# Kernel optimization log

Measured on AMD Instinct MI355X. Metric: run time of the kernel, lower is better.

The kernel has to match this reference:

```python
import jax, jax.numpy as jnp
import numpy as np

B, N, EG = 4, 16384, 131072
H, DK, DV, DM = 4, 32, 32, 128


def setup_inputs() -> dict:
    key = jax.random.key(0)
    ks = jax.random.split(key, 12)
    s = 0.05
    return {
        "edge_indices": jax.random.randint(ks[0], (B, 2, EG), 0, N, dtype=jnp.int32),
        "edge_features": jax.random.normal(ks[1], (B, EG, DM), jnp.float32),
        "input_Q": jax.random.normal(ks[2], (B, N, DM), jnp.float32),
        "input_K": jax.random.normal(ks[3], (B, N, DM), jnp.float32),
        "input_V": jax.random.normal(ks[4], (B, N, DM), jnp.float32),
        "W_Q": jax.random.normal(ks[5], (DM, H * DK), jnp.float32) * s,
        "W_K": jax.random.normal(ks[6], (DM, H * DK), jnp.float32) * s,
        "W_V": jax.random.normal(ks[7], (DM, H * DV), jnp.float32) * s,
        "W_E": jax.random.normal(ks[8], (DM, H * DV), jnp.float32) * s,
        "W_fc": jax.random.normal(ks[9], (H * DV, DM), jnp.float32) * s,
        "ln_gamma": jnp.ones((DM,), jnp.float32),
        "ln_beta": jnp.zeros((DM,), jnp.float32),
    }


def _layer_norm(x, g, b, eps=1e-5):
    mu = jnp.mean(x, axis=-1, keepdims=True)
    var = jnp.mean(jnp.square(x - mu), axis=-1, keepdims=True)
    return g * (x - mu) * jax.lax.rsqrt(var + eps) + b


def _proj(x, W, d):
    # [B, T, DM] @ [DM, H*d] -> [B, H, T, d]
    bsz, t, _ = x.shape
    return (x @ W).reshape(bsz, t, H, d).transpose(0, 2, 1, 3)


def reference(edge_indices, edge_features, input_Q, input_K, input_V,
              W_Q, W_K, W_V, W_E, W_fc, ln_gamma, ln_beta):
    residual = input_Q
    bsz, n_nodes, _ = input_Q.shape
    Q = _proj(input_Q, W_Q, DK)        # [B,H,N,dk]
    K = _proj(input_K, W_K, DK)
    V = _proj(input_V, W_V, DV)
    E = _proj(edge_features, W_E, DV)  # [B,H,Eg,dv]

    inv_sqrt_dk = 1.0 / np.sqrt(DK).astype(np.float32)

    def one_graph(Qb, Kb, Vb, Eb, idx):
        src, tgt = idx[0], idx[1]                       # [Eg]
        Qe = Qb[:, src]                                  # [H,Eg,dk]
        Ke = Kb[:, tgt]
        Ve = Vb[:, tgt]
        scores = (Qe * Ke) * inv_sqrt_dk * Eb            # [H,Eg,dv]
        attn = jnp.exp(jnp.clip(scores.sum(-1, keepdims=True), -5.0, 5.0))  # [H,Eg,1]
        msg = attn * Ve                                  # [H,Eg,dv]
        num = jnp.zeros((H, n_nodes, DV), Qb.dtype).at[:, src].add(msg)
        den = jnp.zeros((H, n_nodes, 1), Qb.dtype).at[:, src].add(attn)
        return num / (den + 1e-8), attn

    out, attn = jax.vmap(one_graph)(Q, K, V, E, edge_indices)  # [B,H,N,dv], [B,H,Eg,1]

    out = out.transpose(0, 2, 1, 3).reshape(bsz, n_nodes, H * DV)
    out = out @ W_fc
    out = _layer_norm(out + residual, ln_gamma, ln_beta)
    # torch code returns attn from the last batch iteration (leading dim 1)
    return out, attn[-1:]
```

## Files before the change

kernel.cpp:

```cpp
#include <hip/hip_runtime.h>

#define BB 4
#define NN 16384
#define EGc 131072
#define CAP 64
#define INVSQ 0.17677669529663687f

typedef unsigned int uint;
typedef unsigned short ushort;
typedef short short8 __attribute__((ext_vector_type(8)));
typedef float floatx4 __attribute__((ext_vector_type(4)));

__device__ __forceinline__ float bflo(uint u) { return __uint_as_float(u << 16); }
__device__ __forceinline__ float bfhi(uint u) { return __uint_as_float(u & 0xffff0000u); }
__device__ __forceinline__ ushort f2bf(float f) {
    uint u = __float_as_uint(f);
    u += 0x7fffu + ((u >> 16) & 1u);
    return (ushort)(u >> 16);
}

#define SA_STRIDE 136
#define SW_STRIDE 136
#define SY_STRIDE 132
struct __align__(16) SMem {
    union {
        struct {
            ushort sA[64 * SA_STRIDE];
            ushort sW[128 * SW_STRIDE];
        };
        float  sY[64 * SY_STRIDE];
        ushort sOut[64 * 128];
    };
};

__device__ __forceinline__ void stage_x512(SMem& sm, const float4* __restrict__ X4,
                                           size_t r0, int t) {
#pragma unroll
    for (int i = 0; i < 4; ++i) {
        int f = t + 512 * i;
        int r = f >> 5, c4 = f & 31;
        float4 x = X4[(r0 + r) * 32 + c4];
        ushort4 h;
        h.x = f2bf(x.x); h.y = f2bf(x.y); h.z = f2bf(x.z); h.w = f2bf(x.w);
        *(ushort4*)&sm.sA[r * SA_STRIDE + c4 * 4] = h;
    }
}

__device__ __forceinline__ void stage_wt512(SMem& sm, const uint4* __restrict__ Wt4, int t) {
#pragma unroll
    for (int i = 0; i < 4; ++i) {
        int f = t + 512 * i;
        int c = f >> 4, kc = f & 15;
        uint4 w = Wt4[f];
        *(uint4*)&sm.sW[c * SW_STRIDE + kc * 8] = w;
    }
}

__device__ __forceinline__ void mfma_core512(const SMem& sm, int t, floatx4 (&acc)[4]) {
    int lane = t & 63, w = t >> 6;
    int wr = (w >> 1) * 16, wc = (w & 1) * 64;
    int m = lane & 15, q = lane >> 4;
#pragma unroll
    for (int ks = 0; ks < 4; ++ks) {
        int k = ks * 32 + q * 8;
        short8 a = *(const short8*)&sm.sA[(wr + m) * SA_STRIDE + k];
#pragma unroll
        for (int j = 0; j < 4; ++j) {
            short8 b = *(const short8*)&sm.sW[(wc + j * 16 + m) * SW_STRIDE + k];
            acc[j] = __builtin_amdgcn_mfma_f32_16x16x32_bf16(a, b, acc[j], 0, 0, 0);
        }
    }
}

__device__ __forceinline__ void acc_zero4(floatx4 (&acc)[4]) {
    floatx4 z = {0.f, 0.f, 0.f, 0.f};
#pragma unroll
    for (int j = 0; j < 4; ++j) acc[j] = z;
}

__device__ __forceinline__ void acc_to_sy512(SMem& sm, int t, const floatx4 (&acc)[4]) {
    int lane = t & 63, w = t >> 6;
    int wr = (w >> 1) * 16, wc = (w & 1) * 64;
    int m = lane & 15, q = lane >> 4;
#pragma unroll
    for (int j = 0; j < 4; ++j)
#pragma unroll
        for (int r = 0; r < 4; ++r)
            sm.sY[(wr + q * 4 + r) * SY_STRIDE + wc + j * 16 + m] = acc[j][r];
}

__global__ __launch_bounds__(256) void transpose_w(const float* __restrict__ W0,
                                                   const float* __restrict__ W1,
                                                   const float* __restrict__ W2,
                                                   const float* __restrict__ W3,
                                                   const float* __restrict__ W4,
                                                   ushort* __restrict__ Wt) {
    __shared__ ushort sT[128 * 136];
    int bi = blockIdx.x;
    const float* W = bi == 0 ? W0 : bi == 1 ? W1 : bi == 2 ? W2 : bi == 3 ? W3 : W4;
    int t = threadIdx.x;
    const float4* Wp = (const float4*)W;
#pragma unroll
    for (int i = 0; i < 16; ++i) {
        int f = t + 256 * i;
        int d = f >> 5, c4 = f & 31;
        float4 w = Wp[f];
        sT[(c4 * 4 + 0) * 136 + d] = f2bf(w.x);
        sT[(c4 * 4 + 1) * 136 + d] = f2bf(w.y);
        sT[(c4 * 4 + 2) * 136 + d] = f2bf(w.z);
        sT[(c4 * 4 + 3) * 136 + d] = f2bf(w.w);
    }
    __syncthreads();
    uint4* out = (uint4*)(Wt + (size_t)bi * 16384);
#pragma unroll
    for (int i = 0; i < 8; ++i) {
        int f = t + 256 * i;
        int c = f >> 4, kc = f & 15;
        out[f] = *(const uint4*)&sT[c * 136 + kc * 8];
    }
}

__global__ __launch_bounds__(512, 6) void proj_mfma(const float* __restrict__ IQ,
                                                    const float* __restrict__ IK,
                                                    const float* __restrict__ IV,
                                                    const ushort* __restrict__ WtAll,
                                                    ushort* __restrict__ Qp,
                                                    ushort* __restrict__ Kp,
                                                    ushort* __restrict__ Vp) {
    __shared__ SMem sm;
    int t = threadIdx.x;
    const float* X; const ushort* Wt; ushort* Y;
    if (blockIdx.y == 0)      { X = IQ; Wt = WtAll;         Y = Qp; }
    else if (blockIdx.y == 1) { X = IK; Wt = WtAll + 16384; Y = Kp; }
    else                      { X = IV; Wt = WtAll + 32768; Y = Vp; }
    size_t r0 = (size_t)blockIdx.x * 64;
    stage_x512(sm, (const float4*)X, r0, t);
    stage_wt512(sm, (const uint4*)Wt, t);
    __syncthreads();
    floatx4 acc[4];
    acc_zero4(acc);
    mfma_core512(sm, t, acc);
    __syncthreads();
    {
        int lane = t & 63, w = t >> 6;
        int wr = (w >> 1) * 16, wc = (w & 1) * 64;
        int m = lane & 15, q = lane >> 4;
#pragma unroll
        for (int j = 0; j < 4; ++j)
#pragma unroll
            for (int r = 0; r < 4; ++r)
                sm.sOut[(wr + q * 4 + r) * 128 + wc + j * 16 + m] = f2bf(acc[j][r]);
    }
    __syncthreads();
    uint4* Y4 = (uint4*)Y;
#pragma unroll
    for (int i = 0; i < 2; ++i) {
        int f = t + 512 * i;
        Y4[r0 * 16 + f] = *(const uint4*)&sm.sOut[f * 8];
    }
}

__global__ __launch_bounds__(512, 6) void edge_kernel(const int* __restrict__ EI,
                                                      const float* __restrict__ EF,
                                                      const ushort* __restrict__ WtE,
                                                      const ushort* __restrict__ Qp,
                                                      const ushort* __restrict__ Kp,
                                                      float* __restrict__ aArr,
                                                      int* __restrict__ list,
                                                      int* __restrict__ cnt,
                                                      float* __restrict__ attn_out) {
    __shared__ SMem sm;
    int t = threadIdx.x;
    int b = blockIdx.x >> 11;
    int tile = blockIdx.x & 2047;
    int e0 = tile * 64;
    int w = t >> 6, lane = t & 63;

    if (t < 64) {
        int ge = e0 + t;
        int src = EI[(size_t)b * 2 * EGc + ge];
        int tgt = EI[(size_t)b * 2 * EGc + EGc + ge];
        int slot = atomicAdd(&cnt[b * NN + src], 1);
        if (slot < CAP) list[((size_t)(b * NN + src)) * CAP + slot] = (tgt << 17) | ge;
    }

    int e8 = w * 8 + (lane & 7);
    int srcv = EI[(size_t)b * 2 * EGc + e0 + e8];
    int tgtv = EI[(size_t)b * 2 * EGc + EGc + e0 + e8];
    const uint* Qu = (const uint*)Qp;
    const uint* Ku = (const uint*)Kp;
    uint q01[8], k01[8];
#pragma unroll
    for (int ei = 0; ei < 8; ++ei) {
        int s = __shfl(srcv, ei, 8);
        int g = __shfl(tgtv, ei, 8);
        q01[ei] = Qu[((size_t)b * NN + s) * 64 + lane];
        k01[ei] = Ku[((size_t)b * NN + g) * 64 + lane];
    }

    stage_x512(sm, (const float4*)EF, (size_t)b * EGc + e0, t);
    stage_wt512(sm, (const uint4*)WtE, t);
    __syncthreads();
    floatx4 acc[4];
    acc_zero4(acc);
    mfma_core512(sm, t, acc);
    __syncthreads();
    acc_to_sy512(sm, t, acc);
    __syncthreads();

    int h = lane >> 4;
    bool isLast = (b == BB - 1);
#pragma unroll
    for (int ei = 0; ei < 8; ++ei) {
        int e = w * 8 + ei;
        float2 ev = *(const float2*)&sm.sY[e * SY_STRIDE + 2 * lane];
        float p = bflo(q01[ei]) * bflo(k01[ei]) * ev.x + bfhi(q01[ei]) * bfhi(k01[ei]) * ev.y;
        p += __shfl_xor(p, 8, 64);
        p += __shfl_xor(p, 4, 64);
        p += __shfl_xor(p, 2, 64);
        p += __shfl_xor(p, 1, 64);
        float av = __expf(fminf(fmaxf(p * INVSQ, -5.f), 5.f));
        int ge = e0 + e;
        if ((lane & 15) == 0) {
            aArr[((size_t)b * EGc + ge) * 4 + h] = av;
            if (isLast) attn_out[(size_t)h * EGc + ge] = av;
        }
    }
}

__global__ __launch_bounds__(256) void gather_kernel(const ushort* __restrict__ Vp,
                                                     const float* __restrict__ aArr,
                                                     const int* __restrict__ list,
                                                     const int* __restrict__ cnt,
                                                     uint* __restrict__ Xg) {
    int t = threadIdx.x;
    int w = t >> 6, lane = t & 63;
    int wid = blockIdx.x * 4 + w;
    size_t n0 = (size_t)wid * 4;
    int b = (int)(n0 >> 14);
    int h = lane >> 4;
    const uint* Vu = (const uint*)Vp;
    const float* aBase = aArr + (size_t)b * EGc * 4;

    int degv = 0;
    if (lane < 4) degv = cnt[n0 + lane];

    for (int ni = 0; ni < 4; ++ni) {
        size_t grow = n0 + ni;
        int deg = __shfl(degv, ni, 64);
        deg = deg < CAP ? deg : CAP;
        int le = 0, tv = 0;
        if (lane < deg) {
            int pk = list[grow * CAP + lane];
            le = pk & 0x1FFFF;
            tv = pk >> 17;
        }
        float afp0, afp1 = 0.f, afp2 = 0.f, afp3 = 0.f;
        {
            int m0 = __shfl(le, lane & 15, 64);
            afp0 = aBase[(size_t)m0 * 4 + h];
            if (deg > 16) { int m1 = __shfl(le, 16 + (lane & 15), 64); afp1 = aBase[(size_t)m1 * 4 + h]; }
            if (deg > 32) { int m2 = __shfl(le, 32 + (lane & 15), 64); afp2 = aBase[(size_t)m2 * 4 + h]; }
            if (deg > 48) { int m3 = __shfl(le, 48 + (lane & 15), 64); afp3 = aBase[(size_t)m3 * 4 + h]; }
        }
        float n0v = 0.f, n1v = 0.f, dh = 0.f;
#define FCHUNK(K, AFP) \
        if (deg > 16 * K) { \
            int lim = deg - 16 * K; lim = lim > 16 ? 16 : lim; \
            _Pragma("unroll 8") \
            for (int j2 = 0; j2 < lim; ++j2) { \
                int tgt = __shfl(tv, 16 * K + j2, 64); \
                float af = __shfl(AFP, (lane & 48) + j2, 64); \
                uint v01 = Vu[((size_t)b * NN + tgt) * 64 + lane]; \
                n0v += af * bflo(v01); n1v += af * bfhi(v01); dh += af; \
            } \
        }
        FCHUNK(0, afp0)
        FCHUNK(1, afp1)
        FCHUNK(2, afp2)
        FCHUNK(3, afp3)
#undef FCHUNK
        float inv = 1.f / (dh + 1e-8f);
        uint packed = (uint)f2bf(n0v * inv) | ((uint)f2bf(n1v * inv) << 16);
        Xg[grow * 64 + lane] = packed;
    }
}

__global__ __launch_bounds__(512, 6) void fc_ln_kernel(const uint* __restrict__ Xg,
                                                       const ushort* __restrict__ WtFC,
                                                       const float* __restrict__ IQ,
                                                       const float* __restrict__ G,
                                                       const float* __restrict__ Bt,
                                                       float* __restrict__ Out) {
    __shared__ SMem sm;
    int t = threadIdx.x;
    size_t r0 = (size_t)blockIdx.x * 64;
    const uint4* X4 = (const uint4*)(Xg + r0 * 64);
#pragma unroll
    for (int i = 0; i < 2; ++i) {
        int f = t + 512 * i;
        int r = f >> 4, c = f & 15;
        uint4 x = X4[f];
        *(uint4*)&sm.sA[r * SA_STRIDE + c * 8] = x;
    }
    stage_wt512(sm, (const uint4*)WtFC, t);
    __syncthreads();
    floatx4 acc[4];
    acc_zero4(acc);
    mfma_core512(sm, t, acc);
    __syncthreads();
    acc_to_sy512(sm, t, acc);
    __syncthreads();

    int w = t >> 6, lane = t & 63;
    float g0 = G[lane], g1 = G[lane + 64];
    float be0 = Bt[lane], be1 = Bt[lane + 64];
    for (int ei = 0; ei < 8; ++ei) {
        int e = w * 8 + ei;
        size_t row = r0 + e;
        float y0 = sm.sY[e * SY_STRIDE + lane]      + IQ[row * 128 + lane];
        float y1 = sm.sY[e * SY_STRIDE + lane + 64] + IQ[row * 128 + lane + 64];
        float s = y0 + y1;
        float qq = y0 * y0 + y1 * y1;
#pragma unroll
        for (int off = 32; off >= 1; off >>= 1) {
            s  += __shfl_xor(s, off, 64);
            qq += __shfl_xor(qq, off, 64);
        }
        float mu = s * (1.f / 128.f);
        float var = qq * (1.f / 128.f) - mu * mu;
        float rstd = rsqrtf(var + 1e-5f);
        Out[row * 128 + lane]      = g0 * (y0 - mu) * rstd + be0;
        Out[row * 128 + lane + 64] = g1 * (y1 - mu) * rstd + be1;
    }
}

extern "C" void kernel_launch(void* const* d_in, const int* in_sizes, int n_in,
                              void* d_out, int out_size, void* d_ws, size_t ws_size,
                              hipStream_t stream) {
    const int*   EI  = (const int*)d_in[0];
    const float* EF  = (const float*)d_in[1];
    const float* IQ  = (const float*)d_in[2];
    const float* IK  = (const float*)d_in[3];
    const float* IV  = (const float*)d_in[4];
    const float* WQ  = (const float*)d_in[5];
    const float* WK  = (const float*)d_in[6];
    const float* WV  = (const float*)d_in[7];
    const float* WE  = (const float*)d_in[8];
    const float* WFC = (const float*)d_in[9];
    const float* G   = (const float*)d_in[10];
    const float* Bt  = (const float*)d_in[11];

    char* ws = (char*)d_ws;
    ushort* Qp   = (ushort*)ws;
    ushort* Kp   = (ushort*)(ws + 16777216);
    ushort* Vp   = (ushort*)(ws + 2 * 16777216);
    ushort* Wt   = (ushort*)(ws + 3 * 16777216);
    float*  aArr = (float*) (ws + 3 * 16777216 + 262144);
    int*    list = (int*)   (ws + 3 * 16777216 + 262144 + 8388608);
    int*    cnt  = (int*)   (ws + 4 * 16777216 + 262144 + 8388608);

    float* out0 = (float*)d_out;
    float* attn_out = out0 + (size_t)BB * NN * 128;

    hipMemsetAsync(cnt, 0, (size_t)BB * NN * sizeof(int), stream);

    transpose_w<<<5, 256, 0, stream>>>(WQ, WK, WV, WE, WFC, Wt);

    dim3 pg(1024, 3);
    proj_mfma<<<pg, 512, 0, stream>>>(IQ, IK, IV, Wt, Qp, Kp, Vp);

    edge_kernel<<<BB * (EGc / 64), 512, 0, stream>>>(EI, EF, Wt + 3 * 16384,
                                                     Qp, Kp, aArr, list, cnt, attn_out);

    uint* Xg = (uint*)Qp;
    gather_kernel<<<4096, 256, 0, stream>>>(Vp, aArr, list, cnt, Xg);

    fc_ln_kernel<<<1024, 512, 0, stream>>>(Xg, Wt + 4 * 16384, IQ, G, Bt, out0);
}
```

Before: 558.6 us.

## Compute edge scores directly from MFMA accumulators with register-held weights

```diff
diff --git a/kernel.cpp b/kernel.cpp
--- a/kernel.cpp
+++ b/kernel.cpp
@@ -160,6 +160,11 @@
     }
 }
 
+struct __align__(16) EdgeSMem {
+    ushort sA[64 * SA_STRIDE];
+    float  sP[8 * 64];
+};
+
 __global__ __launch_bounds__(512, 6) void edge_kernel(const int* __restrict__ EI,
                                                       const float* __restrict__ EF,
                                                       const ushort* __restrict__ WtE,
@@ -169,62 +174,85 @@
                                                       int* __restrict__ list,
                                                       int* __restrict__ cnt,
                                                       float* __restrict__ attn_out) {
-    __shared__ SMem sm;
+    __shared__ EdgeSMem es;
     int t = threadIdx.x;
     int b = blockIdx.x >> 11;
     int tile = blockIdx.x & 2047;
     int e0 = tile * 64;
     int w = t >> 6, lane = t & 63;
+    int m = lane & 15, q = lane >> 4;
+
+    int srcv = EI[(size_t)b * 2 * EGc + e0 + lane];
+    int tgtv = EI[(size_t)b * 2 * EGc + EGc + e0 + lane];
+
+    short8 wf[4];
+#pragma unroll
+    for (int ks = 0; ks < 4; ++ks)
+        wf[ks] = *(const short8*)&WtE[(size_t)(16 * w + m) * 128 + ks * 32 + q * 8];
+
+    const uint2* Qu2 = (const uint2*)Qp;
+    const uint2* Ku2 = (const uint2*)Kp;
+    int cidx = 4 * w + q;
+    uint2 qv[4], kv[4];
+#pragma unroll
+    for (int j = 0; j < 4; ++j) {
+        int s = __shfl(srcv, j * 16 + m, 64);
+        int g = __shfl(tgtv, j * 16 + m, 64);
+        qv[j] = Qu2[((size_t)b * NN + s) * 32 + cidx];
+        kv[j] = Ku2[((size_t)b * NN + g) * 32 + cidx];
+    }
 
     if (t < 64) {
-        int ge = e0 + t;
-        int src = EI[(size_t)b * 2 * EGc + ge];
-        int tgt = EI[(size_t)b * 2 * EGc + EGc + ge];
-        int slot = atomicAdd(&cnt[b * NN + src], 1);
-        if (slot < CAP) list[((size_t)(b * NN + src)) * CAP + slot] = (tgt << 17) | ge;
-    }
-
-    int e8 = w * 8 + (lane & 7);
-    int srcv = EI[(size_t)b * 2 * EGc + e0 + e8];
-    int tgtv = EI[(size_t)b * 2 * EGc + EGc + e0 + e8];
-    const uint* Qu = (const uint*)Qp;
-    const uint* Ku = (const uint*)Kp;
-    uint q01[8], k01[8];
-#pragma unroll
-    for (int ei = 0; ei < 8; ++ei) {
-        int s = __shfl(srcv, ei, 8);
-        int g = __shfl(tgtv, ei, 8);
-        q01[ei] = Qu[((size_t)b * NN + s) * 64 + lane];
-        k01[ei] = Ku[((size_t)b * NN + g) * 64 + lane];
-    }
-
-    stage_x512(sm, (const float4*)EF, (size_t)b * EGc + e0, t);
-    stage_wt512(sm, (const uint4*)WtE, t);
-    __syncthreads();
+        int slot = atomicAdd(&cnt[b * NN + srcv], 1);
+        if (slot < CAP) list[((size_t)(b * NN + srcv)) * CAP + slot] = (tgtv << 17) | (e0 + t);
+    }
+
+    {
+        const float4* X4 = (const float4*)EF;
+        size_t r0 = (size_t)b * EGc + e0;
+#pragma unroll
+        for (int i = 0; i < 4; ++i) {
+            int f = t + 512 * i;
+            int r = f >> 5, c4 = f & 31;
+            float4 x = X4[(r0 + r) * 32 + c4];
+            ushort4 hh;
+            hh.x = f2bf(x.x); hh.y = f2bf(x.y); hh.z = f2bf(x.z); hh.w = f2bf(x.w);
+            *(ushort4*)&es.sA[r * SA_STRIDE + c4 * 4] = hh;
+        }
+    }
+    __syncthreads();
+
     floatx4 acc[4];
     acc_zero4(acc);
-    mfma_core512(sm, t, acc);
-    __syncthreads();
-    acc_to_sy512(sm, t, acc);
-    __syncthreads();
-
-    int h = lane >> 4;
-    bool isLast = (b == BB - 1);
-#pragma unroll
-    for (int ei = 0; ei < 8; ++ei) {
-        int e = w * 8 + ei;
-        float2 ev = *(const float2*)&sm.sY[e * SY_STRIDE + 2 * lane];
-        float p = bflo(q01[ei]) * bflo(k01[ei]) * ev.x + bfhi(q01[ei]) * bfhi(k01[ei]) * ev.y;
-        p += __shfl_xor(p, 8, 64);
-        p += __shfl_xor(p, 4, 64);
-        p += __shfl_xor(p, 2, 64);
-        p += __shfl_xor(p, 1, 64);
-        float av = __expf(fminf(fmaxf(p * INVSQ, -5.f), 5.f));
+#pragma unroll
+    for (int ks = 0; ks < 4; ++ks) {
+        int k = ks * 32 + q * 8;
+#pragma unroll
+        for (int j = 0; j < 4; ++j) {
+            short8 ef = *(const short8*)&es.sA[(j * 16 + m) * SA_STRIDE + k];
+            acc[j] = __builtin_amdgcn_mfma_f32_16x16x32_bf16(wf[ks], ef, acc[j], 0, 0, 0);
+        }
+    }
+
+#pragma unroll
+    for (int j = 0; j < 4; ++j) {
+        float s = bflo(qv[j].x) * bflo(kv[j].x) * acc[j][0]
+                + bfhi(qv[j].x) * bfhi(kv[j].x) * acc[j][1]
+                + bflo(qv[j].y) * bflo(kv[j].y) * acc[j][2]
+                + bfhi(qv[j].y) * bfhi(kv[j].y) * acc[j][3];
+        s += __shfl_xor(s, 16, 64);
+        s += __shfl_xor(s, 32, 64);
+        if (q == 0) es.sP[w * 64 + j * 16 + m] = s;
+    }
+    __syncthreads();
+
+    if (t < 256) {
+        int e = t & 63, h = t >> 6;
+        float sum = es.sP[(2 * h) * 64 + e] + es.sP[(2 * h + 1) * 64 + e];
+        float av = __expf(fminf(fmaxf(sum * INVSQ, -5.f), 5.f));
         int ge = e0 + e;
-        if ((lane & 15) == 0) {
-            aArr[((size_t)b * EGc + ge) * 4 + h] = av;
-            if (isLast) attn_out[(size_t)h * EGc + ge] = av;
-        }
+        aArr[((size_t)b * EGc + ge) * 4 + h] = av;
+        if (b == BB - 1) attn_out[(size_t)h * EGc + ge] = av;
     }
 }
 
```

Measured after the change: 584.2 us. 4.6% more time.
